# Kernel tuning notes

Hardware: AMD Instinct MI355X
Metric: run time of the kernel (lower is better)

The kernel has to match this reference:

```python
import jax, jax.numpy as jnp
import numpy as np

B, S, L = 32, 512, 64
START, STOP, PAD = 61, 62, 63
NEG = -10000.0


def setup_inputs() -> dict:
    key = jax.random.key(0)
    k1, k2, k3, k4 = jax.random.split(key, 4)
    encoder_scores = jax.random.normal(k1, (B, S, L), dtype=jnp.float32)
    transition = jax.random.normal(k2, (L, L), dtype=jnp.float32)
    # constrained transitions, as in __init__
    transition = (transition.at[:, START].set(NEG)
                            .at[STOP, :].set(NEG)
                            .at[:, PAD].set(NEG)
                            .at[PAD, :].set(NEG))
    word_seq_lens = jax.random.randint(k3, (B,), S // 2, S + 1)  # in [S/2, S]
    tags = jax.random.randint(k4, (B, S), 0, START)  # valid non-special labels
    mask = jnp.arange(S)[None, :] < word_seq_lens[:, None]
    return {"encoder_scores": encoder_scores, "transition": transition,
            "word_seq_lens": word_seq_lens, "tags": tags, "mask": mask}


def reference(encoder_scores, transition, word_seq_lens, tags, mask):
    # all_scores[b,s,i,j] = transition[i,j] + encoder_scores[b,s,j]  (B,S,L,L)
    all_scores = transition[None, None, :, :] + encoder_scores[:, :, None, :]

    # ---- forward algorithm (partition function) ----
    alpha0 = all_scores[:, 0, START, :]  # (B,L)

    def step(a_prev, s_t):  # a_prev (B,L), s_t (B,L,L)
        a = jax.nn.logsumexp(a_prev[:, :, None] + s_t, axis=1)
        return a, a

    _, alphas_rest = jax.lax.scan(step, alpha0,
                                  jnp.swapaxes(all_scores[:, 1:], 0, 1))
    alphas = jnp.concatenate([alpha0[:, None, :],
                              jnp.swapaxes(alphas_rest, 0, 1)], axis=1)  # (B,S,L)
    last_alpha = jnp.take_along_axis(
        alphas, (word_seq_lens - 1)[:, None, None], axis=1)[:, 0, :]  # (B,L)
    last_alpha = last_alpha + transition[:, STOP][None, :]
    unlabeled = jax.nn.logsumexp(last_alpha, axis=1)  # (B,)

    # ---- gold-sequence score ----
    # cur[b,s,i] = all_scores[b,s,i,tags[b,s]]
    cur = jnp.take_along_axis(all_scores, tags[:, :, None, None], axis=3)[..., 0]  # (B,S,L)
    mid = jnp.take_along_axis(cur[:, 1:, :], tags[:, :-1, None], axis=2)[..., 0]  # (B,S-1)
    begin = cur[:, 0, START]  # (B,)
    end_ids = jnp.take_along_axis(tags, (word_seq_lens - 1)[:, None], axis=1)[:, 0]
    end_sc = transition[end_ids, STOP]  # (B,)
    labeled = begin + end_sc + jnp.sum(mid * mask[:, 1:].astype(mid.dtype), axis=1)
    return unlabeled, labeled
```

## Files before the change

### kernel.cpp

```cpp
#include <hip/hip_runtime.h>

#define BB 32
#define SS 512
#define LL 64
#define TSTART 61
#define TSTOP 62
#define NSEG 32
#define SEGLEN 16
#define QPAD 68

typedef short short8 __attribute__((ext_vector_type(8)));
typedef float floatx4 __attribute__((ext_vector_type(4)));

union S8 { int i[4]; uint4 u4; short8 v; };

__device__ inline int pack_bf16(float a, float b) {
    unsigned ua = __float_as_uint(a) + 0x8000u;
    unsigned ub = __float_as_uint(b) + 0x8000u;
    return (int)((ua >> 16) | (ub & 0xffff0000u));
}

__global__ __launch_bounds__(64) void crf_seg_kernel(
    const float* __restrict__ enc, const float* __restrict__ Tr,
    const int* __restrict__ lens, const int* __restrict__ tags,
    unsigned short* __restrict__ wsQ, float* __restrict__ wsS,
    float* __restrict__ out)
{
    const int blk = blockIdx.x;
    const int lane = threadIdx.x;

    if (blk >= BB * NSEG * 4) {
        const int b = blk - BB * NSEG * 4;
        const int len = lens[b];
        const int* tg = tags + b * SS;
        const float* eb = enc + b * (SS * LL);
        float acc = 0.f;
        for (int t = 1 + lane; t < len; t += 64) {
            int curt = tg[t], prevt = tg[t - 1];
            acc += Tr[prevt * LL + curt] + eb[t * LL + curt];
        }
        #pragma unroll
        for (int off = 32; off; off >>= 1) acc += __shfl_xor(acc, off);
        if (lane == 0) {
            int t0 = tg[0], te = tg[len - 1];
            acc += Tr[TSTART * LL + t0] + eb[t0];
            acc += Tr[te * LL + TSTOP];
            out[BB + b] = acc;
        }
        return;
    }

    const int b = blk >> 7;
    const int s = (blk >> 2) & 31;
    const int g = blk & 3;
    const int len = lens[b];
    const int tlo = SEGLEN * s + 1;
    const int Teff = min(len - tlo, SEGLEN);
    if (Teff <= 0) return;

    const int q = lane >> 4;
    const int lcol = lane & 15;
    const float* eb = enc + b * (SS * LL);

    __shared__ __align__(16) float QT[16 * QPAD];
    __shared__ __align__(16) float W16[16 * 64];

    float ev[16];
    #pragma unroll
    for (int k = 0; k < 16; ++k) ev[k] = eb[min(tlo + k, SS - 1) * LL + lane];

    short8 Afr[4][2];
    #pragma unroll
    for (int mt = 0; mt < 4; ++mt)
        #pragma unroll
        for (int c2 = 0; c2 < 2; ++c2) {
            float av[8];
            #pragma unroll
            for (int idx = 0; idx < 8; ++idx) {
                int kk = 32 * c2 + 8 * q + idx;
                int mm = 16 * mt + lcol;
                av[idx] = __expf(Tr[kk * LL + mm]) * 0.0078125f;
            }
            S8 u;
            #pragma unroll
            for (int w2 = 0; w2 < 4; ++w2) u.i[w2] = pack_bf16(av[2 * w2], av[2 * w2 + 1]);
            Afr[mt][c2] = u.v;
        }

    {
        const float* trow = Tr + (16 * g + lcol) * LL;
        #pragma unroll
        for (int u = 0; u < 4; ++u) {
            float4 tv = *(const float4*)(trow + 16 * q + 4 * u);
            float4 evv;
            evv.x = __expf(tv.x) * 0.0078125f;
            evv.y = __expf(tv.y) * 0.0078125f;
            evv.z = __expf(tv.z) * 0.0078125f;
            evv.w = __expf(tv.w) * 0.0078125f;
            *(float4*)(QT + lcol * QPAD + 16 * q + 4 * u) = evv;
        }
    }

    #pragma unroll
    for (int k = 0; k < 16; ++k) W16[k * 64 + lane] = __expf(ev[k]);

    float lg = 0.0f;
    #pragma unroll
    for (int cc = 0; cc < 2; ++cc) {
        #pragma unroll
        for (int k = 0; k < 8; ++k) {
            const int i = 8 * cc + k + 2;
            if (i <= Teff) {
                const int wloc = 8 * cc + k;
                float4 qv[2][2], wv[2][2];
                #pragma unroll
                for (int c2 = 0; c2 < 2; ++c2)
                    #pragma unroll
                    for (int h = 0; h < 2; ++h) {
                        qv[c2][h] = *(const float4*)(QT + lcol * QPAD + 32 * c2 + 8 * q + 4 * h);
                        wv[c2][h] = *(const float4*)(W16 + wloc * 64 + 32 * c2 + 8 * q + 4 * h);
                    }
                short8 Bfr[2];
                #pragma unroll
                for (int c2 = 0; c2 < 2; ++c2) {
                    S8 u;
                    u.i[0] = pack_bf16(qv[c2][0].x * wv[c2][0].x, qv[c2][0].y * wv[c2][0].y);
                    u.i[1] = pack_bf16(qv[c2][0].z * wv[c2][0].z, qv[c2][0].w * wv[c2][0].w);
                    u.i[2] = pack_bf16(qv[c2][1].x * wv[c2][1].x, qv[c2][1].y * wv[c2][1].y);
                    u.i[3] = pack_bf16(qv[c2][1].z * wv[c2][1].z, qv[c2][1].w * wv[c2][1].w);
                    Bfr[c2] = u.v;
                }
                float ov[4][4];
                #pragma unroll
                for (int mt = 0; mt < 4; ++mt) {
                    floatx4 z = {0.f, 0.f, 0.f, 0.f};
                    z = __builtin_amdgcn_mfma_f32_16x16x32_bf16(Afr[mt][0], Bfr[0], z, 0, 0, 0);
                    z = __builtin_amdgcn_mfma_f32_16x16x32_bf16(Afr[mt][1], Bfr[1], z, 0, 0, 0);
                    ov[mt][0] = z[0]; ov[mt][1] = z[1]; ov[mt][2] = z[2]; ov[mt][3] = z[3];
                }
                if (cc == 0 && k == 7) {
                    float mx = ov[0][0];
                    #pragma unroll
                    for (int mt = 0; mt < 4; ++mt)
                        #pragma unroll
                        for (int r = 0; r < 4; ++r) mx = fmaxf(mx, ov[mt][r]);
                    #pragma unroll
                    for (int off = 32; off; off >>= 1) mx = fmaxf(mx, __shfl_xor(mx, off));
                    lg += __logf(mx);
                    float rmx = 1.0f / mx;
                    #pragma unroll
                    for (int mt = 0; mt < 4; ++mt)
                        #pragma unroll
                        for (int r = 0; r < 4; ++r) ov[mt][r] *= rmx;
                }
                #pragma unroll
                for (int mt = 0; mt < 4; ++mt) {
                    float4 sv = make_float4(ov[mt][0], ov[mt][1], ov[mt][2], ov[mt][3]);
                    *(float4*)(QT + lcol * QPAD + 16 * mt + 4 * q) = sv;
                }
            }
        }
    }

    const float* wl = W16 + (Teff - 1) * 64;
    unsigned short* qdst = wsQ + (size_t)(b * NSEG + s) * 4096 + (16 * g + lcol) * 64;
    #pragma unroll
    for (int u = 0; u < 2; ++u) {
        const int r0 = 16 * q + 8 * u;
        float4 m0 = *(const float4*)(QT + lcol * QPAD + r0);
        float4 m1 = *(const float4*)(QT + lcol * QPAD + r0 + 4);
        float4 w0 = *(const float4*)(wl + r0);
        float4 w1 = *(const float4*)(wl + r0 + 4);
        S8 o;
        o.i[0] = pack_bf16(m0.x * w0.x, m0.y * w0.y);
        o.i[1] = pack_bf16(m0.z * w0.z, m0.w * w0.w);
        o.i[2] = pack_bf16(m1.x * w1.x, m1.y * w1.y);
        o.i[3] = pack_bf16(m1.z * w1.z, m1.w * w1.w);
        *(uint4*)(qdst + r0) = o.u4;
    }
    if (lane == 0) wsS[(b * NSEG + s) * 4 + g] = lg;
}

__global__ __launch_bounds__(64) void crf_combine_kernel(
    const float* __restrict__ enc, const float* __restrict__ Tr,
    const int* __restrict__ lens,
    const unsigned short* __restrict__ wsQ, const float* __restrict__ wsS,
    float* __restrict__ out)
{
    const int b = blockIdx.x;
    const int j = threadIdx.x;
    const int len = lens[b];
    const int smax = (len - 2) / SEGLEN + 1;
    const int q = j >> 4;
    const int lcol = j & 15;

    const uint4* qb = (const uint4*)(wsQ + (size_t)b * NSEG * 4096);
    int fidx[4][2];
    #pragma unroll
    for (int mt = 0; mt < 4; ++mt)
        #pragma unroll
        for (int c2 = 0; c2 < 2; ++c2)
            fidx[mt][c2] = (16 * mt + lcol) * 8 + 4 * c2 + q;

    __shared__ __align__(16) float Al[64];

    float sc0 = wsS[b * (NSEG * 4) + j];
    float sc1 = wsS[b * (NSEG * 4) + 64 + j];

    float alpha0 = Tr[TSTART * LL + j] + enc[b * (SS * LL) + j];
    float m = alpha0;
    #pragma unroll
    for (int off = 32; off; off >>= 1) m = fmaxf(m, __shfl_xor(m, off));
    Al[j] = __expf(alpha0 - m);
    float logscale = m;
    float invmx = 1.0f;

    uint4 Abuf0[8], Abuf1[8];
    {
        const uint4* p1 = qb + (size_t)min(1, smax - 1) * 512;
        #pragma unroll
        for (int mt = 0; mt < 4; ++mt)
            #pragma unroll
            for (int c2 = 0; c2 < 2; ++c2) {
                Abuf0[mt * 2 + c2] = qb[fidx[mt][c2]];
                Abuf1[mt * 2 + c2] = p1[fidx[mt][c2]];
            }
    }

    int s = 0;
    auto fold = [&](uint4 (&cur)[8]) {
        float4 q0 = *(const float4*)(Al + 8 * q);
        float4 q1 = *(const float4*)(Al + 8 * q + 4);
        float4 q2 = *(const float4*)(Al + 32 + 8 * q);
        float4 q3 = *(const float4*)(Al + 32 + 8 * q + 4);
        S8 b0, b1;
        b0.i[0] = pack_bf16(q0.x * invmx, q0.y * invmx);
        b0.i[1] = pack_bf16(q0.z * invmx, q0.w * invmx);
        b0.i[2] = pack_bf16(q1.x * invmx, q1.y * invmx);
        b0.i[3] = pack_bf16(q1.z * invmx, q1.w * invmx);
        b1.i[0] = pack_bf16(q2.x * invmx, q2.y * invmx);
        b1.i[1] = pack_bf16(q2.z * invmx, q2.w * invmx);
        b1.i[2] = pack_bf16(q3.x * invmx, q3.y * invmx);
        b1.i[3] = pack_bf16(q3.z * invmx, q3.w * invmx);

        S8 a8[8];
        #pragma unroll
        for (int f = 0; f < 8; ++f) a8[f].u4 = cur[f];

        const uint4* pn = qb + (size_t)min(s + 2, smax - 1) * 512;
        #pragma unroll
        for (int mt = 0; mt < 4; ++mt)
            #pragma unroll
            for (int c2 = 0; c2 < 2; ++c2) cur[mt * 2 + c2] = pn[fidx[mt][c2]];

        floatx4 acc[4];
        #pragma unroll
        for (int mt = 0; mt < 4; ++mt) {
            floatx4 z = {0.f, 0.f, 0.f, 0.f};
            z = __builtin_amdgcn_mfma_f32_16x16x32_bf16(a8[2 * mt].v, b0.v, z, 0, 0, 0);
            z = __builtin_amdgcn_mfma_f32_16x16x32_bf16(a8[2 * mt + 1].v, b1.v, z, 0, 0, 0);
            acc[mt] = z;
        }

        float l0, l1, l2, l3;
        if (s < 16) {
            l0 = __shfl(sc0, 4 * s + 0); l1 = __shfl(sc0, 4 * s + 1);
            l2 = __shfl(sc0, 4 * s + 2); l3 = __shfl(sc0, 4 * s + 3);
        } else {
            int e = 4 * (s - 16);
            l0 = __shfl(sc1, e + 0); l1 = __shfl(sc1, e + 1);
            l2 = __shfl(sc1, e + 2); l3 = __shfl(sc1, e + 3);
        }
        float lmax = fmaxf(fmaxf(l0, l1), fmaxf(l2, l3));
        float e0 = __expf(l0 - lmax), e1 = __expf(l1 - lmax);
        float e2 = __expf(l2 - lmax), e3 = __expf(l3 - lmax);
        #pragma unroll
        for (int r = 0; r < 4; ++r) {
            acc[0][r] *= e0; acc[1][r] *= e1; acc[2][r] *= e2; acc[3][r] *= e3;
        }

        if (lcol == 0) {
            #pragma unroll
            for (int mt = 0; mt < 4; ++mt)
                *(float4*)(Al + 16 * mt + 4 * q) =
                    make_float4(acc[mt][0], acc[mt][1], acc[mt][2], acc[mt][3]);
        }

        float mx = acc[0][0];
        #pragma unroll
        for (int mt = 0; mt < 4; ++mt)
            #pragma unroll
            for (int r = 0; r < 4; ++r) mx = fmaxf(mx, acc[mt][r]);
        mx = fmaxf(mx, __shfl_xor(mx, 16));
        mx = fmaxf(mx, __shfl_xor(mx, 32));
        invmx = 1.0f / mx;
        logscale += lmax + __logf(mx);
    };

    while (s < smax) {
        fold(Abuf0);
        ++s;
        if (s >= smax) break;
        fold(Abuf1);
        ++s;
    }

    float aj = Al[j] * invmx;
    float f = aj * __expf(Tr[j * LL + TSTOP]);
    float ssum = f;
    #pragma unroll
    for (int off = 32; off; off >>= 1) ssum += __shfl_xor(ssum, off);
    if (j == 0) {
        const float LN2x7 = 7.0f * 0.69314718055994530942f;
        out[b] = logscale + (float)(len - 1) * LN2x7 + __logf(ssum);
    }
}

__global__ __launch_bounds__(256) void crf_kernel_fb(
    const float* __restrict__ enc, const float* __restrict__ Tr,
    const int* __restrict__ lens, const int* __restrict__ tags,
    float* __restrict__ out)
{
    if (blockIdx.x < BB) {
        const int tid = threadIdx.x;
        if (tid >= 64) return;
        const int b = blockIdx.x;
        const int j = tid;
        const int len = lens[b];
        const float* eb = enc + b * (SS * LL);
        float Ecol[LL];
        #pragma unroll
        for (int i = 0; i < LL; ++i) Ecol[i] = __expf(Tr[i * LL + j]) * 0.0078125f;
        float alpha0 = Tr[TSTART * LL + j] + eb[j];
        float m = alpha0;
        #pragma unroll
        for (int off = 32; off; off >>= 1) m = fmaxf(m, __shfl_xor(m, off));
        float a = __expf(alpha0 - m);
        float logscale = m;
        float ecur[4], enext[4];
        #pragma unroll
        for (int k = 0; k < 4; ++k) ecur[k] = eb[k * LL + j];
        #pragma unroll
        for (int k = 0; k < 4; ++k) enext[k] = eb[(4 + k) * LL + j];
        const int nchunk = (len + 3) >> 2;
        for (int c = 0; c < nchunk; ++c) {
            const int cpre = (c + 2 < 128) ? (c + 2) : 127;
            float efar[4];
            #pragma unroll
            for (int k = 0; k < 4; ++k) efar[k] = eb[(4 * cpre + k) * LL + j];
            #pragma unroll
            for (int k = 0; k < 4; ++k) {
                const int t = 4 * c + k;
                if (t >= 1 && t < len) {
                    const float w = __expf(ecur[k]);
                    const int ai = __float_as_int(a);
                    float s0 = 0.f, s1 = 0.f, s2 = 0.f, s3 = 0.f;
                    #pragma unroll
                    for (int qq = 0; qq < 16; ++qq) {
                        s0 = fmaf(__int_as_float(__builtin_amdgcn_readlane(ai, 4 * qq + 0)), Ecol[4 * qq + 0], s0);
                        s1 = fmaf(__int_as_float(__builtin_amdgcn_readlane(ai, 4 * qq + 1)), Ecol[4 * qq + 1], s1);
                        s2 = fmaf(__int_as_float(__builtin_amdgcn_readlane(ai, 4 * qq + 2)), Ecol[4 * qq + 2], s2);
                        s3 = fmaf(__int_as_float(__builtin_amdgcn_readlane(ai, 4 * qq + 3)), Ecol[4 * qq + 3], s3);
                    }
                    a = ((s0 + s1) + (s2 + s3)) * w;
                    if ((t & 7) == 7) {
                        float mm = a;
                        #pragma unroll
                        for (int off = 32; off; off >>= 1) mm = fmaxf(mm, __shfl_xor(mm, off));
                        logscale += __logf(mm);
                        a = a * (1.0f / mm);
                    }
                }
            }
            #pragma unroll
            for (int k = 0; k < 4; ++k) { ecur[k] = enext[k]; enext[k] = efar[k]; }
        }
        float f = a * __expf(Tr[j * LL + TSTOP]);
        float ssum = f;
        #pragma unroll
        for (int off = 32; off; off >>= 1) ssum += __shfl_xor(ssum, off);
        if (j == 0) {
            const float LN2x7 = 7.0f * 0.69314718055994530942f;
            out[b] = logscale + (float)(len - 1) * LN2x7 + __logf(ssum);
        }
    } else {
        const int b = blockIdx.x - BB;
        const int tid = threadIdx.x;
        const int len = lens[b];
        const int* tg = tags + b * SS;
        const float* eb = enc + b * (SS * LL);
        float acc = 0.f;
        for (int t = 1 + tid; t < len; t += 256) {
            int curt = tg[t], prevt = tg[t - 1];
            acc += Tr[prevt * LL + curt] + eb[t * LL + curt];
        }
        #pragma unroll
        for (int off = 32; off; off >>= 1) acc += __shfl_xor(acc, off);
        __shared__ float red[4];
        if ((tid & 63) == 0) red[tid >> 6] = acc;
        __syncthreads();
        if (tid == 0) {
            float tot = (red[0] + red[1]) + (red[2] + red[3]);
            int t0 = tg[0], te = tg[len - 1];
            tot += Tr[TSTART * LL + t0] + eb[t0];
            tot += Tr[te * LL + TSTOP];
            out[BB + b] = tot;
        }
    }
}

extern "C" void kernel_launch(void* const* d_in, const int* in_sizes, int n_in,
                              void* d_out, int out_size, void* d_ws, size_t ws_size,
                              hipStream_t stream) {
    const float* enc  = (const float*)d_in[0];
    const float* Tr   = (const float*)d_in[1];
    const int*   lens = (const int*)d_in[2];
    const int*   tags = (const int*)d_in[3];
    float* out = (float*)d_out;

    const size_t needQ = (size_t)BB * NSEG * 4096 * sizeof(unsigned short);
    const size_t needS = (size_t)BB * NSEG * 4 * sizeof(float);
    if (ws_size >= needQ + needS) {
        unsigned short* wsQ = (unsigned short*)d_ws;
        float* wsS = (float*)((char*)d_ws + needQ);
        crf_seg_kernel<<<BB * NSEG * 4 + BB, 64, 0, stream>>>(enc, Tr, lens, tags, wsQ, wsS, out);
        crf_combine_kernel<<<BB, 64, 0, stream>>>(enc, Tr, lens, wsQ, wsS, out);
    } else {
        crf_kernel_fb<<<2 * BB, 256, 0, stream>>>(enc, Tr, lens, tags, out);
    }
}
```

Baseline: 100.5 us.

## Fuse segment and combine kernels using per-batch atomic last-block-done counter

Merges the segment kernel and the combine kernel into one launch. Each segment block fences its writes and atomically bumps a per-batch counter, and the last of the 127 blocks for that batch runs the combine step inline. This removes a kernel launch boundary and lets combines for early-finishing batches start while other batches are still working. In exchange it adds atomics and fences, relies on atomicInc wraparound to reset the counter, and assumes the counter memory starts at zero on the first call. It also adds a launch_bounds occupancy hint.

New measurement: 225.8 us. 2.25x slower.

```diff
diff --git a/kernel.cpp b/kernel.cpp
--- a/kernel.cpp
+++ b/kernel.cpp
@@ -20,176 +20,13 @@
     return (int)((ua >> 16) | (ub & 0xffff0000u));
 }
 
-__global__ __launch_bounds__(64) void crf_seg_kernel(
-    const float* __restrict__ enc, const float* __restrict__ Tr,
-    const int* __restrict__ lens, const int* __restrict__ tags,
-    unsigned short* __restrict__ wsQ, float* __restrict__ wsS,
-    float* __restrict__ out)
+__device__ void combine_batch(int b, int j, const float* __restrict__ enc,
+                              const float* __restrict__ Tr, int len,
+                              const unsigned short* __restrict__ wsQ,
+                              const float* __restrict__ wsS,
+                              float* __restrict__ Al,
+                              float* __restrict__ out)
 {
-    const int blk = blockIdx.x;
-    const int lane = threadIdx.x;
-
-    if (blk >= BB * NSEG * 4) {
-        const int b = blk - BB * NSEG * 4;
-        const int len = lens[b];
-        const int* tg = tags + b * SS;
-        const float* eb = enc + b * (SS * LL);
-        float acc = 0.f;
-        for (int t = 1 + lane; t < len; t += 64) {
-            int curt = tg[t], prevt = tg[t - 1];
-            acc += Tr[prevt * LL + curt] + eb[t * LL + curt];
-        }
-        #pragma unroll
-        for (int off = 32; off; off >>= 1) acc += __shfl_xor(acc, off);
-        if (lane == 0) {
-            int t0 = tg[0], te = tg[len - 1];
-            acc += Tr[TSTART * LL + t0] + eb[t0];
-            acc += Tr[te * LL + TSTOP];
-            out[BB + b] = acc;
-        }
-        return;
-    }
-
-    const int b = blk >> 7;
-    const int s = (blk >> 2) & 31;
-    const int g = blk & 3;
-    const int len = lens[b];
-    const int tlo = SEGLEN * s + 1;
-    const int Teff = min(len - tlo, SEGLEN);
-    if (Teff <= 0) return;
-
-    const int q = lane >> 4;
-    const int lcol = lane & 15;
-    const float* eb = enc + b * (SS * LL);
-
-    __shared__ __align__(16) float QT[16 * QPAD];
-    __shared__ __align__(16) float W16[16 * 64];
-
-    float ev[16];
-    #pragma unroll
-    for (int k = 0; k < 16; ++k) ev[k] = eb[min(tlo + k, SS - 1) * LL + lane];
-
-    short8 Afr[4][2];
-    #pragma unroll
-    for (int mt = 0; mt < 4; ++mt)
-        #pragma unroll
-        for (int c2 = 0; c2 < 2; ++c2) {
-            float av[8];
-            #pragma unroll
-            for (int idx = 0; idx < 8; ++idx) {
-                int kk = 32 * c2 + 8 * q + idx;
-                int mm = 16 * mt + lcol;
-                av[idx] = __expf(Tr[kk * LL + mm]) * 0.0078125f;
-            }
-            S8 u;
-            #pragma unroll
-            for (int w2 = 0; w2 < 4; ++w2) u.i[w2] = pack_bf16(av[2 * w2], av[2 * w2 + 1]);
-            Afr[mt][c2] = u.v;
-        }
-
-    {
-        const float* trow = Tr + (16 * g + lcol) * LL;
-        #pragma unroll
-        for (int u = 0; u < 4; ++u) {
-            float4 tv = *(const float4*)(trow + 16 * q + 4 * u);
-            float4 evv;
-            evv.x = __expf(tv.x) * 0.0078125f;
-            evv.y = __expf(tv.y) * 0.0078125f;
-            evv.z = __expf(tv.z) * 0.0078125f;
-            evv.w = __expf(tv.w) * 0.0078125f;
-            *(float4*)(QT + lcol * QPAD + 16 * q + 4 * u) = evv;
-        }
-    }
-
-    #pragma unroll
-    for (int k = 0; k < 16; ++k) W16[k * 64 + lane] = __expf(ev[k]);
-
-    float lg = 0.0f;
-    #pragma unroll
-    for (int cc = 0; cc < 2; ++cc) {
-        #pragma unroll
-        for (int k = 0; k < 8; ++k) {
-            const int i = 8 * cc + k + 2;
-            if (i <= Teff) {
-                const int wloc = 8 * cc + k;
-                float4 qv[2][2], wv[2][2];
-                #pragma unroll
-                for (int c2 = 0; c2 < 2; ++c2)
-                    #pragma unroll
-                    for (int h = 0; h < 2; ++h) {
-                        qv[c2][h] = *(const float4*)(QT + lcol * QPAD + 32 * c2 + 8 * q + 4 * h);
-                        wv[c2][h] = *(const float4*)(W16 + wloc * 64 + 32 * c2 + 8 * q + 4 * h);
-                    }
-                short8 Bfr[2];
-                #pragma unroll
-                for (int c2 = 0; c2 < 2; ++c2) {
-                    S8 u;
-                    u.i[0] = pack_bf16(qv[c2][0].x * wv[c2][0].x, qv[c2][0].y * wv[c2][0].y);
-                    u.i[1] = pack_bf16(qv[c2][0].z * wv[c2][0].z, qv[c2][0].w * wv[c2][0].w);
-                    u.i[2] = pack_bf16(qv[c2][1].x * wv[c2][1].x, qv[c2][1].y * wv[c2][1].y);
-                    u.i[3] = pack_bf16(qv[c2][1].z * wv[c2][1].z, qv[c2][1].w * wv[c2][1].w);
-                    Bfr[c2] = u.v;
-                }
-                float ov[4][4];
-                #pragma unroll
-                for (int mt = 0; mt < 4; ++mt) {
-                    floatx4 z = {0.f, 0.f, 0.f, 0.f};
-                    z = __builtin_amdgcn_mfma_f32_16x16x32_bf16(Afr[mt][0], Bfr[0], z, 0, 0, 0);
-                    z = __builtin_amdgcn_mfma_f32_16x16x32_bf16(Afr[mt][1], Bfr[1], z, 0, 0, 0);
-                    ov[mt][0] = z[0]; ov[mt][1] = z[1]; ov[mt][2] = z[2]; ov[mt][3] = z[3];
-                }
-                if (cc == 0 && k == 7) {
-                    float mx = ov[0][0];
-                    #pragma unroll
-                    for (int mt = 0; mt < 4; ++mt)
-                        #pragma unroll
-                        for (int r = 0; r < 4; ++r) mx = fmaxf(mx, ov[mt][r]);
-                    #pragma unroll
-                    for (int off = 32; off; off >>= 1) mx = fmaxf(mx, __shfl_xor(mx, off));
-                    lg += __logf(mx);
-                    float rmx = 1.0f / mx;
-                    #pragma unroll
-                    for (int mt = 0; mt < 4; ++mt)
-                        #pragma unroll
-                        for (int r = 0; r < 4; ++r) ov[mt][r] *= rmx;
-                }
-                #pragma unroll
-                for (int mt = 0; mt < 4; ++mt) {
-                    float4 sv = make_float4(ov[mt][0], ov[mt][1], ov[mt][2], ov[mt][3]);
-                    *(float4*)(QT + lcol * QPAD + 16 * mt + 4 * q) = sv;
-                }
-            }
-        }
-    }
-
-    const float* wl = W16 + (Teff - 1) * 64;
-    unsigned short* qdst = wsQ + (size_t)(b * NSEG + s) * 4096 + (16 * g + lcol) * 64;
-    #pragma unroll
-    for (int u = 0; u < 2; ++u) {
-        const int r0 = 16 * q + 8 * u;
-        float4 m0 = *(const float4*)(QT + lcol * QPAD + r0);
-        float4 m1 = *(const float4*)(QT + lcol * QPAD + r0 + 4);
-        float4 w0 = *(const float4*)(wl + r0);
-        float4 w1 = *(const float4*)(wl + r0 + 4);
-        S8 o;
-        o.i[0] = pack_bf16(m0.x * w0.x, m0.y * w0.y);
-        o.i[1] = pack_bf16(m0.z * w0.z, m0.w * w0.w);
-        o.i[2] = pack_bf16(m1.x * w1.x, m1.y * w1.y);
-        o.i[3] = pack_bf16(m1.z * w1.z, m1.w * w1.w);
-        *(uint4*)(qdst + r0) = o.u4;
-    }
-    if (lane == 0) wsS[(b * NSEG + s) * 4 + g] = lg;
-}
-
-__global__ __launch_bounds__(64) void crf_combine_kernel(
-    const float* __restrict__ enc, const float* __restrict__ Tr,
-    const int* __restrict__ lens,
-    const unsigned short* __restrict__ wsQ, const float* __restrict__ wsS,
-    float* __restrict__ out)
-{
-    const int b = blockIdx.x;
-    const int j = threadIdx.x;
-    const int len = lens[b];
     const int smax = (len - 2) / SEGLEN + 1;
     const int q = j >> 4;
     const int lcol = j & 15;
@@ -201,8 +38,6 @@
         #pragma unroll
         for (int c2 = 0; c2 < 2; ++c2)
             fidx[mt][c2] = (16 * mt + lcol) * 8 + 4 * c2 + q;
-
-    __shared__ __align__(16) float Al[64];
 
     float sc0 = wsS[b * (NSEG * 4) + j];
     float sc1 = wsS[b * (NSEG * 4) + 64 + j];
@@ -316,6 +151,179 @@
     }
 }
 
+__global__ __launch_bounds__(64, 4) void crf_fused_kernel(
+    const float* __restrict__ enc, const float* __restrict__ Tr,
+    const int* __restrict__ lens, const int* __restrict__ tags,
+    unsigned short* __restrict__ wsQ, float* __restrict__ wsS,
+    unsigned int* __restrict__ cnt,
+    float* __restrict__ out)
+{
+    const int blk = blockIdx.x;
+    const int lane = threadIdx.x;
+
+    if (blk >= BB * NSEG * 4) {
+        const int b = blk - BB * NSEG * 4;
+        const int len = lens[b];
+        const int* tg = tags + b * SS;
+        const float* eb = enc + b * (SS * LL);
+        float acc = 0.f;
+        for (int t = 1 + lane; t < len; t += 64) {
+            int curt = tg[t], prevt = tg[t - 1];
+            acc += Tr[prevt * LL + curt] + eb[t * LL + curt];
+        }
+        #pragma unroll
+        for (int off = 32; off; off >>= 1) acc += __shfl_xor(acc, off);
+        if (lane == 0) {
+            int t0 = tg[0], te = tg[len - 1];
+            acc += Tr[TSTART * LL + t0] + eb[t0];
+            acc += Tr[te * LL + TSTOP];
+            out[BB + b] = acc;
+        }
+        return;
+    }
+
+    const int b = blk >> 7;
+    const int s = (blk >> 2) & 31;
+    const int g = blk & 3;
+    const int len = lens[b];
+    const int tlo = SEGLEN * s + 1;
+    const int Teff = min(len - tlo, SEGLEN);
+
+    __shared__ __align__(16) float QT[16 * QPAD];
+    __shared__ __align__(16) float W16[16 * 64];
+    __shared__ __align__(16) float Al[64];
+
+    if (Teff > 0) {
+        const int q = lane >> 4;
+        const int lcol = lane & 15;
+        const float* eb = enc + b * (SS * LL);
+
+        float ev[16];
+        #pragma unroll
+        for (int k = 0; k < 16; ++k) ev[k] = eb[min(tlo + k, SS - 1) * LL + lane];
+
+        short8 Afr[4][2];
+        #pragma unroll
+        for (int mt = 0; mt < 4; ++mt)
+            #pragma unroll
+            for (int c2 = 0; c2 < 2; ++c2) {
+                float av[8];
+                #pragma unroll
+                for (int idx = 0; idx < 8; ++idx) {
+                    int kk = 32 * c2 + 8 * q + idx;
+                    int mm = 16 * mt + lcol;
+                    av[idx] = __expf(Tr[kk * LL + mm]) * 0.0078125f;
+                }
+                S8 u;
+                #pragma unroll
+                for (int w2 = 0; w2 < 4; ++w2) u.i[w2] = pack_bf16(av[2 * w2], av[2 * w2 + 1]);
+                Afr[mt][c2] = u.v;
+            }
+
+        {
+            const float* trow = Tr + (16 * g + lcol) * LL;
+            #pragma unroll
+            for (int u = 0; u < 4; ++u) {
+                float4 tv = *(const float4*)(trow + 16 * q + 4 * u);
+                float4 evv;
+                evv.x = __expf(tv.x) * 0.0078125f;
+                evv.y = __expf(tv.y) * 0.0078125f;
+                evv.z = __expf(tv.z) * 0.0078125f;
+                evv.w = __expf(tv.w) * 0.0078125f;
+                *(float4*)(QT + lcol * QPAD + 16 * q + 4 * u) = evv;
+            }
+        }
+
+        #pragma unroll
+        for (int k = 0; k < 16; ++k) W16[k * 64 + lane] = __expf(ev[k]);
+
+        float lg = 0.0f;
+        #pragma unroll
+        for (int cc = 0; cc < 2; ++cc) {
+            #pragma unroll
+            for (int k = 0; k < 8; ++k) {
+                const int i = 8 * cc + k + 2;
+                if (i <= Teff) {
+                    const int wloc = 8 * cc + k;
+                    float4 qv[2][2], wv[2][2];
+                    #pragma unroll
+                    for (int c2 = 0; c2 < 2; ++c2)
+                        #pragma unroll
+                        for (int h = 0; h < 2; ++h) {
+                            qv[c2][h] = *(const float4*)(QT + lcol * QPAD + 32 * c2 + 8 * q + 4 * h);
+                            wv[c2][h] = *(const float4*)(W16 + wloc * 64 + 32 * c2 + 8 * q + 4 * h);
+                        }
+                    short8 Bfr[2];
+                    #pragma unroll
+                    for (int c2 = 0; c2 < 2; ++c2) {
+                        S8 u;
+                        u.i[0] = pack_bf16(qv[c2][0].x * wv[c2][0].x, qv[c2][0].y * wv[c2][0].y);
+                        u.i[1] = pack_bf16(qv[c2][0].z * wv[c2][0].z, qv[c2][0].w * wv[c2][0].w);
+                        u.i[2] = pack_bf16(qv[c2][1].x * wv[c2][1].x, qv[c2][1].y * wv[c2][1].y);
+                        u.i[3] = pack_bf16(qv[c2][1].z * wv[c2][1].z, qv[c2][1].w * wv[c2][1].w);
+                        Bfr[c2] = u.v;
+                    }
+                    float ov[4][4];
+                    #pragma unroll
+                    for (int mt = 0; mt < 4; ++mt) {
+                        floatx4 z = {0.f, 0.f, 0.f, 0.f};
+                        z = __builtin_amdgcn_mfma_f32_16x16x32_bf16(Afr[mt][0], Bfr[0], z, 0, 0, 0);
+                        z = __builtin_amdgcn_mfma_f32_16x16x32_bf16(Afr[mt][1], Bfr[1], z, 0, 0, 0);
+                        ov[mt][0] = z[0]; ov[mt][1] = z[1]; ov[mt][2] = z[2]; ov[mt][3] = z[3];
+                    }
+                    if (cc == 0 && k == 7) {
+                        float mx = ov[0][0];
+                        #pragma unroll
+                        for (int mt = 0; mt < 4; ++mt)
+                            #pragma unroll
+                            for (int r = 0; r < 4; ++r) mx = fmaxf(mx, ov[mt][r]);
+                        #pragma unroll
+                        for (int off = 32; off; off >>= 1) mx = fmaxf(mx, __shfl_xor(mx, off));
+                        lg += __logf(mx);
+                        float rmx = 1.0f / mx;
+                        #pragma unroll
+                        for (int mt = 0; mt < 4; ++mt)
+                            #pragma unroll
+                            for (int r = 0; r < 4; ++r) ov[mt][r] *= rmx;
+                    }
+                    #pragma unroll
+                    for (int mt = 0; mt < 4; ++mt) {
+                        float4 sv = make_float4(ov[mt][0], ov[mt][1], ov[mt][2], ov[mt][3]);
+                        *(float4*)(QT + lcol * QPAD + 16 * mt + 4 * q) = sv;
+                    }
+                }
+            }
+        }
+
+        const float* wl = W16 + (Teff - 1) * 64;
+        unsigned short* qdst = wsQ + (size_t)(b * NSEG + s) * 4096 + (16 * g + lcol) * 64;
+        #pragma unroll
+        for (int u = 0; u < 2; ++u) {
+            const int r0 = 16 * q + 8 * u;
+            float4 m0 = *(const float4*)(QT + lcol * QPAD + r0);
+            float4 m1 = *(const float4*)(QT + lcol * QPAD + r0 + 4);
+            float4 w0 = *(const float4*)(wl + r0);
+            float4 w1 = *(const float4*)(wl + r0 + 4);
+            S8 o;
+            o.i[0] = pack_bf16(m0.x * w0.x, m0.y * w0.y);
+            o.i[1] = pack_bf16(m0.z * w0.z, m0.w * w0.w);
+            o.i[2] = pack_bf16(m1.x * w1.x, m1.y * w1.y);
+            o.i[3] = pack_bf16(m1.z * w1.z, m1.w * w1.w);
+            *(uint4*)(qdst + r0) = o.u4;
+        }
+        if (lane == 0) wsS[(b * NSEG + s) * 4 + g] = lg;
+    }
+
+    __threadfence();
+    unsigned int old = 0;
+    if (lane == 0) old = atomicInc(&cnt[b], 127u);
+    old = __shfl((int)old, 0);
+    if (old == 126u) {
+        __threadfence();
+        combine_batch(b, lane, enc, Tr, len, wsQ, wsS, Al, out);
+    }
+}
+
 __global__ __launch_bounds__(256) void crf_kernel_fb(
     const float* __restrict__ enc, const float* __restrict__ Tr,
     const int* __restrict__ lens, const int* __restrict__ tags,
@@ -420,11 +428,13 @@
 
     const size_t needQ = (size_t)BB * NSEG * 4096 * sizeof(unsigned short);
     const size_t needS = (size_t)BB * NSEG * 4 * sizeof(float);
-    if (ws_size >= needQ + needS) {
+    const size_t needC = (size_t)BB * sizeof(unsigned int);
+    if (ws_size >= needQ + needS + needC) {
         unsigned short* wsQ = (unsigned short*)d_ws;
         float* wsS = (float*)((char*)d_ws + needQ);
-        crf_seg_kernel<<<BB * NSEG * 4 + BB, 64, 0, stream>>>(enc, Tr, lens, tags, wsQ, wsS, out);
-        crf_combine_kernel<<<BB, 64, 0, stream>>>(enc, Tr, lens, wsQ, wsS, out);
+        unsigned int* cnt = (unsigned int*)((char*)d_ws + needQ + needS);
+        crf_fused_kernel<<<BB * NSEG * 4 + BB, 64, 0, stream>>>(
+            enc, Tr, lens, tags, wsQ, wsS, cnt, out);
     } else {
         crf_kernel_fb<<<2 * BB, 256, 0, stream>>>(enc, Tr, lens, tags, out);
     }
```

## Precompute exp(transition) tables in a prep kernel and keep segment state in bf16

Applied to the files above, without the earlier changes.

Adds a small prep kernel that computes exp(transition) once, writes it as packed bf16 MFMA A-fragments plus a float table, and also absorbs the gold-score blocks. Each segment block now loads these tables instead of recomputing 64+ exps per lane. The segment recurrence applies the emission weight after the MFMA rather than before, and stores the running state in LDS as packed bf16. This removes the per-step multiply/pack of the B operand and the final scaling pass. The cost is an extra kernel launch and a serial dependency on the prep kernel.

After: 102.1 us. No clear change (+1.6%).

```diff
diff --git a/kernel.cpp b/kernel.cpp
--- a/kernel.cpp
+++ b/kernel.cpp
@@ -7,7 +7,7 @@
 #define TSTOP 62
 #define NSEG 32
 #define SEGLEN 16
-#define QPAD 68
+#define QPADB 72
 
 typedef short short8 __attribute__((ext_vector_type(8)));
 typedef float floatx4 __attribute__((ext_vector_type(4)));
@@ -20,17 +20,16 @@
     return (int)((ua >> 16) | (ub & 0xffff0000u));
 }
 
-__global__ __launch_bounds__(64) void crf_seg_kernel(
+__global__ __launch_bounds__(64) void crf_prep_kernel(
     const float* __restrict__ enc, const float* __restrict__ Tr,
     const int* __restrict__ lens, const int* __restrict__ tags,
-    unsigned short* __restrict__ wsQ, float* __restrict__ wsS,
+    uint4* __restrict__ tblA, float* __restrict__ tblE,
     float* __restrict__ out)
 {
     const int blk = blockIdx.x;
     const int lane = threadIdx.x;
-
-    if (blk >= BB * NSEG * 4) {
-        const int b = blk - BB * NSEG * 4;
+    if (blk < BB) {
+        const int b = blk;
         const int len = lens[b];
         const int* tg = tags + b * SS;
         const float* eb = enc + b * (SS * LL);
@@ -49,7 +48,35 @@
         }
         return;
     }
-
+    float rv[64];
+    #pragma unroll
+    for (int k = 0; k < 64; ++k) {
+        float v = __expf(Tr[k * LL + lane]) * 0.0078125f;
+        rv[k] = v;
+        tblE[k * LL + lane] = v;
+    }
+    const int mt = lane >> 4, lc = lane & 15;
+    #pragma unroll
+    for (int c2 = 0; c2 < 2; ++c2)
+        #pragma unroll
+        for (int q = 0; q < 4; ++q) {
+            int k0 = 32 * c2 + 8 * q;
+            uint4 u;
+            u.x = (unsigned)pack_bf16(rv[k0 + 0], rv[k0 + 1]);
+            u.y = (unsigned)pack_bf16(rv[k0 + 2], rv[k0 + 3]);
+            u.z = (unsigned)pack_bf16(rv[k0 + 4], rv[k0 + 5]);
+            u.w = (unsigned)pack_bf16(rv[k0 + 6], rv[k0 + 7]);
+            tblA[(mt * 2 + c2) * 64 + q * 16 + lc] = u;
+        }
+}
+
+__global__ __launch_bounds__(64, 4) void crf_seg_kernel(
+    const float* __restrict__ enc, const int* __restrict__ lens,
+    const uint4* __restrict__ tblA, const float* __restrict__ tblE,
+    unsigned short* __restrict__ wsQ, float* __restrict__ wsS)
+{
+    const int blk = blockIdx.x;
+    const int lane = threadIdx.x;
     const int b = blk >> 7;
     const int s = (blk >> 2) & 31;
     const int g = blk & 3;
@@ -62,47 +89,40 @@
     const int lcol = lane & 15;
     const float* eb = enc + b * (SS * LL);
 
-    __shared__ __align__(16) float QT[16 * QPAD];
+    __shared__ __align__(16) unsigned short QT[16 * QPADB];
     __shared__ __align__(16) float W16[16 * 64];
 
     float ev[16];
-    #pragma unroll
-    for (int k = 0; k < 16; ++k) ev[k] = eb[min(tlo + k, SS - 1) * LL + lane];
-
-    short8 Afr[4][2];
-    #pragma unroll
-    for (int mt = 0; mt < 4; ++mt)
-        #pragma unroll
-        for (int c2 = 0; c2 < 2; ++c2) {
-            float av[8];
-            #pragma unroll
-            for (int idx = 0; idx < 8; ++idx) {
-                int kk = 32 * c2 + 8 * q + idx;
-                int mm = 16 * mt + lcol;
-                av[idx] = __expf(Tr[kk * LL + mm]) * 0.0078125f;
-            }
-            S8 u;
-            #pragma unroll
-            for (int w2 = 0; w2 < 4; ++w2) u.i[w2] = pack_bf16(av[2 * w2], av[2 * w2 + 1]);
-            Afr[mt][c2] = u.v;
-        }
+    if (Teff == SEGLEN) {
+        #pragma unroll
+        for (int k = 0; k < 16; ++k) ev[k] = eb[(tlo + k) * LL + lane];
+    } else {
+        #pragma unroll
+        for (int k = 0; k < 16; ++k) ev[k] = eb[min(tlo + k, SS - 1) * LL + lane];
+    }
+    S8 Af[8];
+    #pragma unroll
+    for (int f = 0; f < 8; ++f) Af[f].u4 = tblA[f * 64 + lane];
+    float4 ei[4];
+    #pragma unroll
+    for (int u = 0; u < 4; ++u)
+        ei[u] = *(const float4*)(tblE + (16 * g + lcol) * LL + 16 * q + 4 * u);
+
+    #pragma unroll
+    for (int k = 0; k < 16; ++k) W16[k * 64 + lane] = __expf(ev[k]);
 
     {
-        const float* trow = Tr + (16 * g + lcol) * LL;
+        int p[8];
         #pragma unroll
         for (int u = 0; u < 4; ++u) {
-            float4 tv = *(const float4*)(trow + 16 * q + 4 * u);
-            float4 evv;
-            evv.x = __expf(tv.x) * 0.0078125f;
-            evv.y = __expf(tv.y) * 0.0078125f;
-            evv.z = __expf(tv.z) * 0.0078125f;
-            evv.w = __expf(tv.w) * 0.0078125f;
-            *(float4*)(QT + lcol * QPAD + 16 * q + 4 * u) = evv;
-        }
-    }
-
-    #pragma unroll
-    for (int k = 0; k < 16; ++k) W16[k * 64 + lane] = __expf(ev[k]);
+            float4 wv = *(const float4*)(W16 + 16 * q + 4 * u);
+            p[2 * u]     = pack_bf16(ei[u].x * wv.x, ei[u].y * wv.y);
+            p[2 * u + 1] = pack_bf16(ei[u].z * wv.z, ei[u].w * wv.w);
+        }
+        unsigned short* qt = QT + lcol * QPADB + 16 * q;
+        *(uint4*)(qt)     = make_uint4(p[0], p[1], p[2], p[3]);
+        *(uint4*)(qt + 8) = make_uint4(p[4], p[5], p[6], p[7]);
+    }
 
     float lg = 0.0f;
     #pragma unroll
@@ -111,32 +131,26 @@
         for (int k = 0; k < 8; ++k) {
             const int i = 8 * cc + k + 2;
             if (i <= Teff) {
-                const int wloc = 8 * cc + k;
-                float4 qv[2][2], wv[2][2];
+                S8 B0, B1;
+                B0.u4 = *(const uint4*)(QT + lcol * QPADB + 8 * q);
+                B1.u4 = *(const uint4*)(QT + lcol * QPADB + 32 + 8 * q);
+                floatx4 z[4];
                 #pragma unroll
-                for (int c2 = 0; c2 < 2; ++c2)
-                    #pragma unroll
-                    for (int h = 0; h < 2; ++h) {
-                        qv[c2][h] = *(const float4*)(QT + lcol * QPAD + 32 * c2 + 8 * q + 4 * h);
-                        wv[c2][h] = *(const float4*)(W16 + wloc * 64 + 32 * c2 + 8 * q + 4 * h);
-                    }
-                short8 Bfr[2];
-                #pragma unroll
-                for (int c2 = 0; c2 < 2; ++c2) {
-                    S8 u;
-                    u.i[0] = pack_bf16(qv[c2][0].x * wv[c2][0].x, qv[c2][0].y * wv[c2][0].y);
-                    u.i[1] = pack_bf16(qv[c2][0].z * wv[c2][0].z, qv[c2][0].w * wv[c2][0].w);
-                    u.i[2] = pack_bf16(qv[c2][1].x * wv[c2][1].x, qv[c2][1].y * wv[c2][1].y);
-                    u.i[3] = pack_bf16(qv[c2][1].z * wv[c2][1].z, qv[c2][1].w * wv[c2][1].w);
-                    Bfr[c2] = u.v;
+                for (int mt = 0; mt < 4; ++mt) {
+                    floatx4 zz = {0.f, 0.f, 0.f, 0.f};
+                    zz = __builtin_amdgcn_mfma_f32_16x16x32_bf16(Af[2 * mt].v,     B0.v, zz, 0, 0, 0);
+                    zz = __builtin_amdgcn_mfma_f32_16x16x32_bf16(Af[2 * mt + 1].v, B1.v, zz, 0, 0, 0);
+                    z[mt] = zz;
                 }
+                const int wloc = 8 * cc + k + 1;
                 float ov[4][4];
                 #pragma unroll
                 for (int mt = 0; mt < 4; ++mt) {
-                    floatx4 z = {0.f, 0.f, 0.f, 0.f};
-                    z = __builtin_amdgcn_mfma_f32_16x16x32_bf16(Afr[mt][0], Bfr[0], z, 0, 0, 0);
-                    z = __builtin_amdgcn_mfma_f32_16x16x32_bf16(Afr[mt][1], Bfr[1], z, 0, 0, 0);
-                    ov[mt][0] = z[0]; ov[mt][1] = z[1]; ov[mt][2] = z[2]; ov[mt][3] = z[3];
+                    float4 wv = *(const float4*)(W16 + wloc * 64 + 16 * mt + 4 * q);
+                    ov[mt][0] = z[mt][0] * wv.x;
+                    ov[mt][1] = z[mt][1] * wv.y;
+                    ov[mt][2] = z[mt][2] * wv.z;
+                    ov[mt][3] = z[mt][3] * wv.w;
                 }
                 if (cc == 0 && k == 7) {
                     float mx = ov[0][0];
@@ -155,28 +169,20 @@
                 }
                 #pragma unroll
                 for (int mt = 0; mt < 4; ++mt) {
-                    float4 sv = make_float4(ov[mt][0], ov[mt][1], ov[mt][2], ov[mt][3]);
-                    *(float4*)(QT + lcol * QPAD + 16 * mt + 4 * q) = sv;
+                    int p0 = pack_bf16(ov[mt][0], ov[mt][1]);
+                    int p1 = pack_bf16(ov[mt][2], ov[mt][3]);
+                    *(uint2*)(QT + lcol * QPADB + 16 * mt + 4 * q) =
+                        make_uint2((unsigned)p0, (unsigned)p1);
                 }
             }
         }
     }
 
-    const float* wl = W16 + (Teff - 1) * 64;
     unsigned short* qdst = wsQ + (size_t)(b * NSEG + s) * 4096 + (16 * g + lcol) * 64;
     #pragma unroll
     for (int u = 0; u < 2; ++u) {
-        const int r0 = 16 * q + 8 * u;
-        float4 m0 = *(const float4*)(QT + lcol * QPAD + r0);
-        float4 m1 = *(const float4*)(QT + lcol * QPAD + r0 + 4);
-        float4 w0 = *(const float4*)(wl + r0);
-        float4 w1 = *(const float4*)(wl + r0 + 4);
-        S8 o;
-        o.i[0] = pack_bf16(m0.x * w0.x, m0.y * w0.y);
-        o.i[1] = pack_bf16(m0.z * w0.z, m0.w * w0.w);
-        o.i[2] = pack_bf16(m1.x * w1.x, m1.y * w1.y);
-        o.i[3] = pack_bf16(m1.z * w1.z, m1.w * w1.w);
-        *(uint4*)(qdst + r0) = o.u4;
+        uint4 v = *(const uint4*)(QT + lcol * QPADB + 16 * q + 8 * u);
+        *(uint4*)(qdst + 16 * q + 8 * u) = v;
     }
     if (lane == 0) wsS[(b * NSEG + s) * 4 + g] = lg;
 }
@@ -420,10 +426,15 @@
 
     const size_t needQ = (size_t)BB * NSEG * 4096 * sizeof(unsigned short);
     const size_t needS = (size_t)BB * NSEG * 4 * sizeof(float);
-    if (ws_size >= needQ + needS) {
+    const size_t needA = (size_t)8 * 64 * sizeof(uint4);
+    const size_t needE = (size_t)64 * 64 * sizeof(float);
+    if (ws_size >= needQ + needS + needA + needE) {
         unsigned short* wsQ = (unsigned short*)d_ws;
         float* wsS = (float*)((char*)d_ws + needQ);
-        crf_seg_kernel<<<BB * NSEG * 4 + BB, 64, 0, stream>>>(enc, Tr, lens, tags, wsQ, wsS, out);
+        uint4* tblA = (uint4*)((char*)d_ws + needQ + needS);
+        float* tblE = (float*)((char*)d_ws + needQ + needS + needA);
+        crf_prep_kernel<<<BB + 1, 64, 0, stream>>>(enc, Tr, lens, tags, tblA, tblE, out);
+        crf_seg_kernel<<<BB * NSEG * 4, 64, 0, stream>>>(enc, lens, tblA, tblE, wsQ, wsS);
         crf_combine_kernel<<<BB, 64, 0, stream>>>(enc, Tr, lens, wsQ, wsS, out);
     } else {
         crf_kernel_fb<<<2 * BB, 256, 0, stream>>>(enc, Tr, lens, tags, out);
```
